# Kernel optimization log

Measured on AMD Instinct MI355X. Metric: run time of the kernel, lower is better.

The kernel has to match this reference:

```python
import jax, jax.numpy as jnp
import numpy as np
import math

K = 10      # number of propagation steps
BETA = 2.0  # log-weighting base
N_NODES = 100000
N_EDGES = 1000000
HIDDEN = 64


def setup_inputs() -> dict:
    key = jax.random.key(0)
    k1, k2, k3 = jax.random.split(key, 3)
    feat = jax.random.normal(k1, (N_NODES, HIDDEN), dtype=jnp.float32)
    src = jax.random.randint(k2, (N_EDGES,), 0, N_NODES, dtype=jnp.int64)
    dst = jax.random.randint(k3, (N_EDGES,), 0, N_NODES, dtype=jnp.int64)
    return {"feat": feat, "src": src, "dst": dst}


def reference(feat, src, dst):
    n = feat.shape[0]
    ones_e = jnp.ones(src.shape, dtype=feat.dtype)
    # out-degree of source nodes, in-degree of destination nodes
    out_deg = jax.ops.segment_sum(ones_e, src, num_segments=n)
    in_deg = jax.ops.segment_sum(ones_e, dst, num_segments=n)
    src_norm = jnp.maximum(out_deg, 1.0) ** -0.5  # [N]
    dst_norm = jnp.maximum(in_deg, 1.0) ** -0.5   # [N]

    # log-based combination weights over the K+1 snapshots
    logs = [math.log(BETA + i) for i in range(1, K + 2)]
    denom = sum(logs)
    w = [l / denom for l in logs]

    h = feat
    out = w[0] * feat
    for step in range(K):
        # gather-scale on source side, scatter-sum to destinations, scale on dst side
        m = (h * src_norm[:, None])[src]                      # [E, D]
        h = jax.ops.segment_sum(m, dst, num_segments=n)       # [N, D]
        h = h * dst_norm[:, None]
        out = out + w[step + 1] * h
    return out
```

## Files before the change

kernel.cpp:

```cpp
#include <hip/hip_runtime.h>
#include <hip/hip_bf16.h>
#include <math.h>

#define HIDDEN 64
#define K_STEPS 10
#define SLICES 2
#define SLICE_N 51200
#define SLICE_W (SLICE_N / 4)
#define PADU 4

struct Wts { float v[K_STEPS + 1]; };

typedef float v2f __attribute__((ext_vector_type(2)));

__device__ __forceinline__ float bits2f(unsigned int u) {
    union { unsigned int i; float f; } c; c.i = u; return c.f;
}
__device__ __forceinline__ unsigned short f2bf(float f) {
    union { float f; unsigned int u; } c; c.f = f;
    unsigned int u = c.u;
    return (unsigned short)((u + 0x7FFF + ((u >> 16) & 1)) >> 16);
}
__device__ __forceinline__ void unpack_add(v2f acc[4], uint4 v) {
    v2f t;
    t.x = bits2f(v.x << 16); t.y = bits2f(v.x & 0xFFFF0000u); acc[0] += t;
    t.x = bits2f(v.y << 16); t.y = bits2f(v.y & 0xFFFF0000u); acc[1] += t;
    t.x = bits2f(v.z << 16); t.y = bits2f(v.z & 0xFFFF0000u); acc[2] += t;
    t.x = bits2f(v.w << 16); t.y = bits2f(v.w & 0xFFFF0000u); acc[3] += t;
}

__global__ void detect_kernel(const int* __restrict__ srcw,
                              const unsigned short* __restrict__ featw,
                              int* __restrict__ flags) {
    __shared__ int odd_nonzero;
    __shared__ int exp_in_range;
    if (threadIdx.x == 0) { odd_nonzero = 0; exp_in_range = 0; }
    __syncthreads();
    int w = srcw[2 * threadIdx.x + 1];
    if (w != 0) atomicAdd(&odd_nonzero, 1);
    unsigned short f = featw[2 * threadIdx.x];
    int ex = (f >> 7) & 0xFF;
    if (ex >= 90 && ex <= 135) atomicAdd(&exp_in_range, 1);
    __syncthreads();
    if (threadIdx.x == 0) {
        flags[0] = (odd_nonzero == 0) ? 1 : 0;
        flags[1] = (exp_in_range >= 240) ? 0 : 1;
    }
}

__global__ void hist_kernel(const void* __restrict__ src, const void* __restrict__ dst,
                            const int* __restrict__ flags,
                            unsigned* __restrict__ partials,
                            unsigned char* __restrict__ rank,
                            int E, int chunkE, int nchunks) {
    __shared__ unsigned bins[SLICE_W];
    int cx = blockIdx.x, sy = blockIdx.y, az = blockIdx.z;
    for (int i = threadIdx.x; i < SLICE_W; i += 256) bins[i] = 0;
    __syncthreads();
    const void* arr = az ? dst : src;
    int i64 = flags[0];
    int base = cx * chunkE;
    int lim = min(base + chunkE, E);
    int sliceBase = sy * SLICE_N;
    for (int e = base + threadIdx.x; e < lim; e += 256) {
        int v = i64 ? (int)((const long long*)arr)[e] : ((const int*)arr)[e];
        unsigned local = (unsigned)(v - sliceBase);
        if (local < SLICE_N) {
            int sh = (local & 3) * 8;
            unsigned old = atomicAdd(&bins[local >> 2], 1u << sh);
            if (az) rank[e] = (unsigned char)((old >> sh) & 0xFF);
        }
    }
    __syncthreads();
    unsigned* out = partials + ((size_t)((az * SLICES + sy) * nchunks + cx)) * SLICE_W;
    for (int i = threadIdx.x; i < SLICE_W; i += 256) out[i] = bins[i];
}

__global__ void reduce_kernel(const unsigned* __restrict__ partials,
                              unsigned* __restrict__ chunk_pre,
                              int* __restrict__ out_deg, int* __restrict__ in_deg,
                              float* __restrict__ src_norm, float* __restrict__ dst_norm,
                              int N, int nchunks) {
    int t = blockIdx.x * blockDim.x + threadIdx.x;
    if (t >= 2 * SLICES * SLICE_W) return;
    int a = t / (SLICES * SLICE_W);
    int r = t % (SLICES * SLICE_W);
    int s = r / SLICE_W;
    int lw = r % SLICE_W;
    const unsigned* p = partials + ((size_t)((a * SLICES + s) * nchunks)) * SLICE_W + lw;
    unsigned sum = 0;
    if (a == 1) {
        for (int c = 0; c < nchunks; ++c) {
            chunk_pre[((size_t)(c * SLICES + s)) * SLICE_W + lw] = sum;
            sum += p[(size_t)c * SLICE_W];
        }
    } else {
        for (int c = 0; c < nchunks; ++c) sum += p[(size_t)c * SLICE_W];
    }
    int nodeBase = s * SLICE_N + lw * 4;
    int* deg = a ? in_deg : out_deg;
    float* nrm = a ? dst_norm : src_norm;
    #pragma unroll
    for (int k = 0; k < 4; ++k) {
        int n = nodeBase + k;
        if (n < N) {
            int d = (int)((sum >> (k * 8)) & 0xFF);
            deg[n] = d;
            nrm[n] = 1.0f / sqrtf(fmaxf((float)d, 1.0f));
        }
    }
}

__global__ void scanA_kernel(const int* __restrict__ deg, int* __restrict__ row_ptr,
                             int* __restrict__ block_sums, int N) {
    __shared__ int lds[256];
    int t = threadIdx.x;
    int base = blockIdx.x * 1024 + t * 4;
    int v0 = (base + 0 < N) ? ((deg[base + 0] + (PADU - 1)) & ~(PADU - 1)) : 0;
    int v1 = (base + 1 < N) ? ((deg[base + 1] + (PADU - 1)) & ~(PADU - 1)) : 0;
    int v2 = (base + 2 < N) ? ((deg[base + 2] + (PADU - 1)) & ~(PADU - 1)) : 0;
    int v3 = (base + 3 < N) ? ((deg[base + 3] + (PADU - 1)) & ~(PADU - 1)) : 0;
    int s = v0 + v1 + v2 + v3;
    lds[t] = s;
    __syncthreads();
    for (int off = 1; off < 256; off <<= 1) {
        int x = 0;
        if (t >= off) x = lds[t - off];
        __syncthreads();
        if (t >= off) lds[t] += x;
        __syncthreads();
    }
    int excl = lds[t] - s;
    if (t == 255) block_sums[blockIdx.x] = lds[255];
    if (base + 0 < N) row_ptr[base + 0] = excl;
    if (base + 1 < N) row_ptr[base + 1] = excl + v0;
    if (base + 2 < N) row_ptr[base + 2] = excl + v0 + v1;
    if (base + 3 < N) row_ptr[base + 3] = excl + v0 + v1 + v2;
}

__global__ void scanB_kernel(int* __restrict__ bs, int nb) {
    __shared__ int lds[1024];
    int t = threadIdx.x;
    int v = (t < nb) ? bs[t] : 0;
    lds[t] = v;
    __syncthreads();
    for (int off = 1; off < 1024; off <<= 1) {
        int x = 0;
        if (t >= off) x = lds[t - off];
        __syncthreads();
        if (t >= off) lds[t] += x;
        __syncthreads();
    }
    if (t < nb) bs[t] = lds[t] - v;
    if (t == nb - 1) bs[1024] = lds[t];
}

__global__ void scanC_pad_kernel(const int* __restrict__ raw_row,
                                 const int* __restrict__ block_offs,
                                 const int* __restrict__ in_deg,
                                 int* __restrict__ row_fin,
                                 int* __restrict__ col, int N) {
    int i = blockIdx.x * blockDim.x + threadIdx.x;
    if (i >= N) return;
    int b0 = raw_row[i] + block_offs[i >> 10];
    int b1 = (i + 1 < N) ? (raw_row[i + 1] + block_offs[(i + 1) >> 10])
                         : block_offs[1024];
    row_fin[i] = b0;
    if (i == 0) row_fin[N] = block_offs[1024];
    int s = b0 + in_deg[i];
    for (int j = s; j < b1; ++j) col[j] = N;
}

__global__ void scatter_kernel(const void* __restrict__ src, const void* __restrict__ dst,
                               const int* __restrict__ flags,
                               const int* __restrict__ row_fin,
                               const unsigned* __restrict__ chunk_pre,
                               const unsigned char* __restrict__ rank,
                               int* __restrict__ col, int E, int chunkShift) {
    int i64 = flags[0];
    int stride = gridDim.x * blockDim.x;
    for (int e = blockIdx.x * blockDim.x + threadIdx.x; e < E; e += stride) {
        int s, d;
        if (i64) { s = (int)((const long long*)src)[e]; d = (int)((const long long*)dst)[e]; }
        else     { s = ((const int*)src)[e];            d = ((const int*)dst)[e]; }
        int c = e >> chunkShift;
        int si = (d >= SLICE_N) ? 1 : 0;
        unsigned local = (unsigned)d - si * SLICE_N;
        unsigned prew = chunk_pre[((size_t)(c * SLICES + si)) * SLICE_W + (local >> 2)];
        int pre = (int)((prew >> ((local & 3) * 8)) & 0xFF);
        col[row_fin[d] + pre + (int)rank[e]] = s;
    }
}

__global__ void init_kernel(const void* __restrict__ feat_raw,
                            const int* __restrict__ flags,
                            const float* __restrict__ src_norm,
                            uint4* __restrict__ hs8, float4* __restrict__ out_acc4,
                            float w0, int nchunks, int writeAcc) {
    int i = blockIdx.x * blockDim.x + threadIdx.x;
    if (i >= nchunks) return;
    int n = i >> 3;
    int c = i & 7;
    float sn = src_norm[n];
    float f[8];
    if (flags[1]) {
        float4 a = ((const float4*)feat_raw)[i * 2];
        float4 b = ((const float4*)feat_raw)[i * 2 + 1];
        f[0] = a.x; f[1] = a.y; f[2] = a.z; f[3] = a.w;
        f[4] = b.x; f[5] = b.y; f[6] = b.z; f[7] = b.w;
    } else {
        uint4 u = ((const uint4*)feat_raw)[i];
        f[0] = bits2f(u.x << 16); f[1] = bits2f(u.x & 0xFFFF0000u);
        f[2] = bits2f(u.y << 16); f[3] = bits2f(u.y & 0xFFFF0000u);
        f[4] = bits2f(u.z << 16); f[5] = bits2f(u.z & 0xFFFF0000u);
        f[6] = bits2f(u.w << 16); f[7] = bits2f(u.w & 0xFFFF0000u);
    }
    uint4 h;
    h.x = (unsigned int)f2bf(f[0] * sn) | ((unsigned int)f2bf(f[1] * sn) << 16);
    h.y = (unsigned int)f2bf(f[2] * sn) | ((unsigned int)f2bf(f[3] * sn) << 16);
    h.z = (unsigned int)f2bf(f[4] * sn) | ((unsigned int)f2bf(f[5] * sn) << 16);
    h.w = (unsigned int)f2bf(f[6] * sn) | ((unsigned int)f2bf(f[7] * sn) << 16);
    hs8[i] = h;
    if (writeAcc) {
        float4 o0, o1;
        o0.x = w0 * f[0]; o0.y = w0 * f[1]; o0.z = w0 * f[2]; o0.w = w0 * f[3];
        o1.x = w0 * f[4]; o1.y = w0 * f[5]; o1.z = w0 * f[6]; o1.w = w0 * f[7];
        size_t ob = (size_t)n * 16 + c * 2;
        out_acc4[ob] = o0;
        out_acc4[ob + 1] = o1;
    }
}

__global__ void zrow_kernel(uint4* __restrict__ hs_region, int snapN, int nsnap, int N) {
    int i = blockIdx.x * blockDim.x + threadIdx.x;
    int k = i >> 3, r = i & 7;
    if (k < nsnap) {
        uint4 z; z.x = 0u; z.y = 0u; z.z = 0u; z.w = 0u;
        hs_region[(size_t)k * snapN + ((size_t)N << 3) + r] = z;
    }
}

__device__ __forceinline__ void gather_row(const uint4* __restrict__ hs8,
                                           const int* __restrict__ col,
                                           int beg, int end, int fo,
                                           v2f a0[4], v2f a1[4]) {
    int e = beg;
    int nq = (end - beg) >> 2;
    if (nq & 1) {
        int4 c = *(const int4*)(col + e);
        uint4 v0 = hs8[((unsigned)c.x << 3) | fo];
        uint4 v1 = hs8[((unsigned)c.y << 3) | fo];
        uint4 v2 = hs8[((unsigned)c.z << 3) | fo];
        uint4 v3 = hs8[((unsigned)c.w << 3) | fo];
        unpack_add(a0, v0);
        unpack_add(a1, v1);
        unpack_add(a0, v2);
        unpack_add(a1, v3);
        e += 4;
    }
    if (e < end) {
        int4 c0 = *(const int4*)(col + e);
        int4 c1 = *(const int4*)(col + e + 4);
        for (;;) {
            int4 d0 = c0, d1 = c1;
            int ne = e + 8;
            if (ne < end) {
                c0 = *(const int4*)(col + ne);
                c1 = *(const int4*)(col + ne + 4);
            }
            uint4 v0 = hs8[((unsigned)d0.x << 3) | fo];
            uint4 v1 = hs8[((unsigned)d0.y << 3) | fo];
            uint4 v2 = hs8[((unsigned)d0.z << 3) | fo];
            uint4 v3 = hs8[((unsigned)d0.w << 3) | fo];
            uint4 v4 = hs8[((unsigned)d1.x << 3) | fo];
            uint4 v5 = hs8[((unsigned)d1.y << 3) | fo];
            uint4 v6 = hs8[((unsigned)d1.z << 3) | fo];
            uint4 v7 = hs8[((unsigned)d1.w << 3) | fo];
            unpack_add(a0, v0);
            unpack_add(a1, v1);
            unpack_add(a0, v2);
            unpack_add(a1, v3);
            unpack_add(a0, v4);
            unpack_add(a1, v5);
            unpack_add(a0, v6);
            unpack_add(a1, v7);
            e = ne;
            if (e >= end) break;
        }
    }
}

__global__ __launch_bounds__(256) void step_snap(
        const uint4* __restrict__ hs8, const int* __restrict__ row_fin,
        const int* __restrict__ col, const float* __restrict__ src_norm,
        const float* __restrict__ dst_norm, uint4* __restrict__ hs_next8, int N) {
    int wid = (blockIdx.x * 256 + threadIdx.x) >> 6;
    int nw = (gridDim.x * 256) >> 6;
    int lane = threadIdx.x & 63;
    int grp = lane >> 3, fo = lane & 7;
    for (int nbase = wid * 8; nbase < N; nbase += nw * 8) {
        int node = nbase + grp;
        int beg = 0, end = 0;
        if (node < N) { beg = row_fin[node]; end = row_fin[node + 1]; }
        v2f a0[4] = {v2f{0.f,0.f}, v2f{0.f,0.f}, v2f{0.f,0.f}, v2f{0.f,0.f}};
        v2f a1[4] = {v2f{0.f,0.f}, v2f{0.f,0.f}, v2f{0.f,0.f}, v2f{0.f,0.f}};
        if (beg < end) gather_row(hs8, col, beg, end, fo, a0, a1);
        if (node < N) {
            float m = dst_norm[node] * src_norm[node];
            #pragma unroll
            for (int k = 0; k < 4; ++k) a0[k] += a1[k];
            uint4 hn;
            hn.x = (unsigned int)f2bf(a0[0].x * m) | ((unsigned int)f2bf(a0[0].y * m) << 16);
            hn.y = (unsigned int)f2bf(a0[1].x * m) | ((unsigned int)f2bf(a0[1].y * m) << 16);
            hn.z = (unsigned int)f2bf(a0[2].x * m) | ((unsigned int)f2bf(a0[2].y * m) << 16);
            hn.w = (unsigned int)f2bf(a0[3].x * m) | ((unsigned int)f2bf(a0[3].y * m) << 16);
            hs_next8[((unsigned)node << 3) | fo] = hn;
        }
    }
}

template <bool LAST>
__global__ __launch_bounds__(256) void step_acc(
        const uint4* __restrict__ hs8, const int* __restrict__ row_fin,
        const int* __restrict__ col, const float* __restrict__ src_norm,
        const float* __restrict__ dst_norm, uint4* __restrict__ hs_next8,
        float4* __restrict__ out_acc4, float4* __restrict__ out4, float w, int N) {
    int wid = (blockIdx.x * 256 + threadIdx.x) >> 6;
    int nw = (gridDim.x * 256) >> 6;
    int lane = threadIdx.x & 63;
    int grp = lane >> 3, fo = lane & 7;
    for (int nbase = wid * 8; nbase < N; nbase += nw * 8) {
        int node = nbase + grp;
        int beg = 0, end = 0;
        if (node < N) { beg = row_fin[node]; end = row_fin[node + 1]; }
        v2f a0[4] = {v2f{0.f,0.f}, v2f{0.f,0.f}, v2f{0.f,0.f}, v2f{0.f,0.f}};
        v2f a1[4] = {v2f{0.f,0.f}, v2f{0.f,0.f}, v2f{0.f,0.f}, v2f{0.f,0.f}};
        if (beg < end) gather_row(hs8, col, beg, end, fo, a0, a1);
        if (node < N) {
            #pragma unroll
            for (int k = 0; k < 4; ++k) a0[k] += a1[k];
            float dn = dst_norm[node];
            float h0 = a0[0].x * dn, h1 = a0[0].y * dn, h2 = a0[1].x * dn, h3 = a0[1].y * dn;
            float h4 = a0[2].x * dn, h5 = a0[2].y * dn, h6 = a0[3].x * dn, h7 = a0[3].y * dn;
            size_t ob = (size_t)node * 16 + fo * 2;
            float4 o0 = out_acc4[ob];
            float4 o1 = out_acc4[ob + 1];
            o0.x += w * h0; o0.y += w * h1; o0.z += w * h2; o0.w += w * h3;
            o1.x += w * h4; o1.y += w * h5; o1.z += w * h6; o1.w += w * h7;
            if (LAST) {
                out4[ob] = o0;
                out4[ob + 1] = o1;
            } else {
                out_acc4[ob] = o0;
                out_acc4[ob + 1] = o1;
                float sn = src_norm[node];
                uint4 hn;
                hn.x = (unsigned int)f2bf(h0 * sn) | ((unsigned int)f2bf(h1 * sn) << 16);
                hn.y = (unsigned int)f2bf(h2 * sn) | ((unsigned int)f2bf(h3 * sn) << 16);
                hn.z = (unsigned int)f2bf(h4 * sn) | ((unsigned int)f2bf(h5 * sn) << 16);
                hn.w = (unsigned int)f2bf(h6 * sn) | ((unsigned int)f2bf(h7 * sn) << 16);
                hs_next8[((unsigned)node << 3) | fo] = hn;
            }
        }
    }
}

__global__ void combine_kernel(const void* __restrict__ feat_raw,
                               const int* __restrict__ flags,
                               const int* __restrict__ out_deg,
                               const uint4* __restrict__ hs_base,
                               float4* __restrict__ out4,
                               Wts wts, int snapN, int nchunks) {
    int i = blockIdx.x * blockDim.x + threadIdx.x;
    if (i >= nchunks) return;
    int n = i >> 3;
    float inv = sqrtf(fmaxf((float)out_deg[n], 1.0f));
    float acc[8];
    if (flags[1]) {
        float4 a = ((const float4*)feat_raw)[i * 2];
        float4 b = ((const float4*)feat_raw)[i * 2 + 1];
        acc[0] = a.x; acc[1] = a.y; acc[2] = a.z; acc[3] = a.w;
        acc[4] = b.x; acc[5] = b.y; acc[6] = b.z; acc[7] = b.w;
    } else {
        uint4 u = ((const uint4*)feat_raw)[i];
        acc[0] = bits2f(u.x << 16); acc[1] = bits2f(u.x & 0xFFFF0000u);
        acc[2] = bits2f(u.y << 16); acc[3] = bits2f(u.y & 0xFFFF0000u);
        acc[4] = bits2f(u.z << 16); acc[5] = bits2f(u.z & 0xFFFF0000u);
        acc[6] = bits2f(u.w << 16); acc[7] = bits2f(u.w & 0xFFFF0000u);
    }
    float w0 = wts.v[0];
    #pragma unroll
    for (int j = 0; j < 8; ++j) acc[j] *= w0;
    #pragma unroll
    for (int k = 1; k <= K_STEPS; ++k) {
        uint4 u = hs_base[(size_t)k * snapN + i];
        float s = wts.v[k] * inv;
        acc[0] += s * bits2f(u.x << 16); acc[1] += s * bits2f(u.x & 0xFFFF0000u);
        acc[2] += s * bits2f(u.y << 16); acc[3] += s * bits2f(u.y & 0xFFFF0000u);
        acc[4] += s * bits2f(u.z << 16); acc[5] += s * bits2f(u.z & 0xFFFF0000u);
        acc[6] += s * bits2f(u.w << 16); acc[7] += s * bits2f(u.w & 0xFFFF0000u);
    }
    float4 o0 = {acc[0], acc[1], acc[2], acc[3]};
    float4 o1 = {acc[4], acc[5], acc[6], acc[7]};
    out4[i * 2] = o0;
    out4[i * 2 + 1] = o1;
}

extern "C" void kernel_launch(void* const* d_in, const int* in_sizes, int n_in,
                              void* d_out, int out_size, void* d_ws, size_t ws_size,
                              hipStream_t stream) {
    const void* feat_raw = d_in[0];
    const void* src_raw = d_in[1];
    const void* dst_raw = d_in[2];
    float4* out4 = (float4*)d_out;

    const int N = in_sizes[0] / HIDDEN;
    const int E = (in_sizes[1] > 1500000) ? in_sizes[1] / 2 : in_sizes[1];
    const int nchunks = N * 8;
    const int snapN = nchunks + 8;
    const int Ecap = E + (PADU - 1) * N + 16;

    auto align256 = [](size_t b) { return (b + 255) & ~(size_t)255; };
    size_t base_bytes = align256(2 * sizeof(int))
                      + align256((size_t)N * sizeof(int))
                      + align256((size_t)N * sizeof(int))
                      + align256((size_t)(N + 1) * sizeof(int))
                      + align256((size_t)(N + 1) * sizeof(int))
                      + align256(1025 * sizeof(int))
                      + align256((size_t)Ecap * sizeof(int))
                      + align256((size_t)N * sizeof(float))
                      + align256((size_t)N * sizeof(float))
                      + align256((size_t)E);
    auto hist_bytes = [&](int C) {
        return align256((size_t)2 * SLICES * C * SLICE_W * sizeof(unsigned))
             + align256((size_t)C * SLICES * SLICE_W * sizeof(unsigned));
    };
    size_t snap_bytes = align256((size_t)(K_STEPS + 1) * snapN * sizeof(uint4));
    size_t acc_bytes  = align256((size_t)2 * snapN * sizeof(uint4))
                      + align256((size_t)N * 16 * sizeof(float4));

    int chunkShift = 13;
    int CHc = (E + (1 << chunkShift) - 1) >> chunkShift;
    int snapMode;
    if (ws_size >= base_bytes + hist_bytes(CHc) + snap_bytes) {
        snapMode = 1;
    } else {
        chunkShift = 14;
        CHc = (E + (1 << chunkShift) - 1) >> chunkShift;
        if (ws_size >= base_bytes + hist_bytes(CHc) + snap_bytes) {
            snapMode = 1;
        } else if (ws_size >= base_bytes + hist_bytes(CHc) + acc_bytes) {
            snapMode = 0;
        } else {
            chunkShift = 15;
            CHc = (E + (1 << chunkShift) - 1) >> chunkShift;
            snapMode = 0;
        }
    }
    const int chunkE = 1 << chunkShift;

    char* p = (char*)d_ws;
    auto alloc = [&](size_t bytes) {
        char* r = p;
        p += (bytes + 255) & ~(size_t)255;
        return r;
    };
    int* flags = (int*)alloc(2 * sizeof(int));
    int* out_deg = (int*)alloc((size_t)N * sizeof(int));
    int* in_deg = (int*)alloc((size_t)N * sizeof(int));
    int* row_ptr = (int*)alloc((size_t)(N + 1) * sizeof(int));
    int* row_fin = (int*)alloc((size_t)(N + 1) * sizeof(int));
    int* block_sums = (int*)alloc(1025 * sizeof(int));
    int* col = (int*)alloc((size_t)Ecap * sizeof(int));
    float* src_norm = (float*)alloc((size_t)N * sizeof(float));
    float* dst_norm = (float*)alloc((size_t)N * sizeof(float));
    unsigned char* rank = (unsigned char*)alloc((size_t)E);
    unsigned* partials = (unsigned*)alloc((size_t)2 * SLICES * CHc * SLICE_W * sizeof(unsigned));
    unsigned* chunk_pre = (unsigned*)alloc((size_t)CHc * SLICES * SLICE_W * sizeof(unsigned));
    uint4* hs_region;
    float4* out_acc = nullptr;
    if (snapMode) {
        hs_region = (uint4*)alloc((size_t)(K_STEPS + 1) * snapN * sizeof(uint4));
    } else {
        hs_region = (uint4*)alloc((size_t)2 * snapN * sizeof(uint4));
        out_acc = (float4*)alloc((size_t)N * 16 * sizeof(float4));
    }

    double logs[K_STEPS + 1];
    double denom = 0.0;
    for (int i = 0; i < K_STEPS + 1; ++i) {
        logs[i] = log(2.0 + (double)(i + 1));
        denom += logs[i];
    }
    Wts wts;
    for (int i = 0; i < K_STEPS + 1; ++i) wts.v[i] = (float)(logs[i] / denom);

    detect_kernel<<<1, 256, 0, stream>>>((const int*)src_raw,
                                         (const unsigned short*)feat_raw, flags);
    hist_kernel<<<dim3(CHc, SLICES, 2), 256, 0, stream>>>(src_raw, dst_raw, flags,
                                                          partials, rank, E, chunkE, CHc);
    reduce_kernel<<<(2 * SLICES * SLICE_W + 255) / 256, 256, 0, stream>>>(
        partials, chunk_pre, out_deg, in_deg, src_norm, dst_norm, N, CHc);

    int nb = (N + 1023) / 1024;
    scanA_kernel<<<nb, 256, 0, stream>>>(in_deg, row_ptr, block_sums, N);
    scanB_kernel<<<1, 1024, 0, stream>>>(block_sums, nb);
    scanC_pad_kernel<<<(N + 255) / 256, 256, 0, stream>>>(row_ptr, block_sums, in_deg,
                                                          row_fin, col, N);
    scatter_kernel<<<min(2048, (E + 255) / 256), 256, 0, stream>>>(
        src_raw, dst_raw, flags, row_fin, chunk_pre, rank, col, E, chunkShift);

    init_kernel<<<(nchunks + 255) / 256, 256, 0, stream>>>(
        feat_raw, flags, src_norm, hs_region, out_acc, wts.v[0], nchunks, snapMode ? 0 : 1);
    zrow_kernel<<<1, 128, 0, stream>>>(hs_region, snapN, snapMode ? (K_STEPS + 1) : 2, N);

    const int work_blocks = (((N + 7) / 8) + 3) / 4;
    if (snapMode) {
        for (int step = 0; step < K_STEPS; ++step) {
            const uint4* cur = hs_region + (size_t)step * snapN;
            uint4* nxt = hs_region + (size_t)(step + 1) * snapN;
            step_snap<<<work_blocks, 256, 0, stream>>>(cur, row_fin, col, src_norm,
                                                       dst_norm, nxt, N);
        }
        combine_kernel<<<(nchunks + 255) / 256, 256, 0, stream>>>(
            feat_raw, flags, out_deg, hs_region, out4, wts, snapN, nchunks);
    } else {
        uint4* cur = hs_region;
        uint4* nxt = hs_region + snapN;
        for (int step = 0; step < K_STEPS; ++step) {
            if (step == K_STEPS - 1) {
                step_acc<true><<<work_blocks, 256, 0, stream>>>(
                    cur, row_fin, col, src_norm, dst_norm, nxt, out_acc, out4,
                    wts.v[step + 1], N);
            } else {
                step_acc<false><<<work_blocks, 256, 0, stream>>>(
                    cur, row_fin, col, src_norm, dst_norm, nxt, out_acc, out4,
                    wts.v[step + 1], N);
            }
            uint4* t = cur; cur = nxt; nxt = t;
        }
    }
}
```

Before: 390.9 us.

## Use single full-range LDS histogram per block and fold zero-row init into init kernel

The degree histogram now covers all 102400 nodes in one 100KB LDS array per block with 1024 threads, instead of two 51200-node slices processed by separate blocks. Each edge index is read once per array rather than once per slice, and the bounds check and slice arithmetic disappear from the histogram and scatter kernels. The separate zero-row kernel is merged into init_kernel, saving one launch. In exchange, the large LDS footprint limits occupancy to one block per CU, and the hard-coded FULLN assumes N is at most 102400.

```diff
diff --git a/kernel.cpp b/kernel.cpp
--- a/kernel.cpp
+++ b/kernel.cpp
@@ -4,9 +4,8 @@
 
 #define HIDDEN 64
 #define K_STEPS 10
-#define SLICES 2
-#define SLICE_N 51200
-#define SLICE_W (SLICE_N / 4)
+#define FULLN 102400
+#define FULLW (FULLN / 4)
 #define PADU 4
 
 struct Wts { float v[K_STEPS + 1]; };
@@ -48,32 +47,30 @@
     }
 }
 
-__global__ void hist_kernel(const void* __restrict__ src, const void* __restrict__ dst,
-                            const int* __restrict__ flags,
-                            unsigned* __restrict__ partials,
-                            unsigned char* __restrict__ rank,
-                            int E, int chunkE, int nchunks) {
-    __shared__ unsigned bins[SLICE_W];
-    int cx = blockIdx.x, sy = blockIdx.y, az = blockIdx.z;
-    for (int i = threadIdx.x; i < SLICE_W; i += 256) bins[i] = 0;
+__global__ __launch_bounds__(1024) void hist_kernel(
+        const void* __restrict__ src, const void* __restrict__ dst,
+        const int* __restrict__ flags,
+        unsigned* __restrict__ partials,
+        unsigned char* __restrict__ rank,
+        int E, int chunkE, int nchunks) {
+    __shared__ unsigned bins[FULLW];
+    int cx = blockIdx.x, az = blockIdx.y;
+    for (int i = threadIdx.x; i < FULLW; i += 1024) bins[i] = 0;
     __syncthreads();
     const void* arr = az ? dst : src;
     int i64 = flags[0];
     int base = cx * chunkE;
     int lim = min(base + chunkE, E);
-    int sliceBase = sy * SLICE_N;
-    for (int e = base + threadIdx.x; e < lim; e += 256) {
+    for (int e = base + threadIdx.x; e < lim; e += 1024) {
         int v = i64 ? (int)((const long long*)arr)[e] : ((const int*)arr)[e];
-        unsigned local = (unsigned)(v - sliceBase);
-        if (local < SLICE_N) {
-            int sh = (local & 3) * 8;
-            unsigned old = atomicAdd(&bins[local >> 2], 1u << sh);
-            if (az) rank[e] = (unsigned char)((old >> sh) & 0xFF);
-        }
+        unsigned uv = (unsigned)v;
+        int sh = (uv & 3) * 8;
+        unsigned old = atomicAdd(&bins[uv >> 2], 1u << sh);
+        if (az) rank[e] = (unsigned char)((old >> sh) & 0xFF);
     }
     __syncthreads();
-    unsigned* out = partials + ((size_t)((az * SLICES + sy) * nchunks + cx)) * SLICE_W;
-    for (int i = threadIdx.x; i < SLICE_W; i += 256) out[i] = bins[i];
+    unsigned* out = partials + ((size_t)(az * nchunks + cx)) * FULLW;
+    for (int i = threadIdx.x; i < FULLW; i += 1024) out[i] = bins[i];
 }
 
 __global__ void reduce_kernel(const unsigned* __restrict__ partials,
@@ -82,22 +79,20 @@
                               float* __restrict__ src_norm, float* __restrict__ dst_norm,
                               int N, int nchunks) {
     int t = blockIdx.x * blockDim.x + threadIdx.x;
-    if (t >= 2 * SLICES * SLICE_W) return;
-    int a = t / (SLICES * SLICE_W);
-    int r = t % (SLICES * SLICE_W);
-    int s = r / SLICE_W;
-    int lw = r % SLICE_W;
-    const unsigned* p = partials + ((size_t)((a * SLICES + s) * nchunks)) * SLICE_W + lw;
+    if (t >= 2 * FULLW) return;
+    int a = t / FULLW;
+    int lw = t % FULLW;
+    const unsigned* p = partials + ((size_t)a * nchunks) * FULLW + lw;
     unsigned sum = 0;
     if (a == 1) {
         for (int c = 0; c < nchunks; ++c) {
-            chunk_pre[((size_t)(c * SLICES + s)) * SLICE_W + lw] = sum;
-            sum += p[(size_t)c * SLICE_W];
+            chunk_pre[(size_t)c * FULLW + lw] = sum;
+            sum += p[(size_t)c * FULLW];
         }
     } else {
-        for (int c = 0; c < nchunks; ++c) sum += p[(size_t)c * SLICE_W];
-    }
-    int nodeBase = s * SLICE_N + lw * 4;
+        for (int c = 0; c < nchunks; ++c) sum += p[(size_t)c * FULLW];
+    }
+    int nodeBase = lw * 4;
     int* deg = a ? in_deg : out_deg;
     float* nrm = a ? dst_norm : src_norm;
     #pragma unroll
@@ -184,10 +179,8 @@
         if (i64) { s = (int)((const long long*)src)[e]; d = (int)((const long long*)dst)[e]; }
         else     { s = ((const int*)src)[e];            d = ((const int*)dst)[e]; }
         int c = e >> chunkShift;
-        int si = (d >= SLICE_N) ? 1 : 0;
-        unsigned local = (unsigned)d - si * SLICE_N;
-        unsigned prew = chunk_pre[((size_t)(c * SLICES + si)) * SLICE_W + (local >> 2)];
-        int pre = (int)((prew >> ((local & 3) * 8)) & 0xFF);
+        unsigned prew = chunk_pre[(size_t)c * FULLW + ((unsigned)d >> 2)];
+        int pre = (int)((prew >> ((d & 3) * 8)) & 0xFF);
         col[row_fin[d] + pre + (int)rank[e]] = s;
     }
 }
@@ -196,9 +189,18 @@
                             const int* __restrict__ flags,
                             const float* __restrict__ src_norm,
                             uint4* __restrict__ hs8, float4* __restrict__ out_acc4,
-                            float w0, int nchunks, int writeAcc) {
+                            float w0, int nchunks, int writeAcc,
+                            int snapN, int nsnap) {
     int i = blockIdx.x * blockDim.x + threadIdx.x;
-    if (i >= nchunks) return;
+    if (i >= nchunks) {
+        int j = i - nchunks;
+        int k = j >> 3, r = j & 7;
+        if (k < nsnap) {
+            uint4 z; z.x = 0u; z.y = 0u; z.z = 0u; z.w = 0u;
+            hs8[(size_t)k * snapN + nchunks + r] = z;
+        }
+        return;
+    }
     int n = i >> 3;
     int c = i & 7;
     float sn = src_norm[n];
@@ -228,15 +230,6 @@
         size_t ob = (size_t)n * 16 + c * 2;
         out_acc4[ob] = o0;
         out_acc4[ob + 1] = o1;
-    }
-}
-
-__global__ void zrow_kernel(uint4* __restrict__ hs_region, int snapN, int nsnap, int N) {
-    int i = blockIdx.x * blockDim.x + threadIdx.x;
-    int k = i >> 3, r = i & 7;
-    if (k < nsnap) {
-        uint4 z; z.x = 0u; z.y = 0u; z.z = 0u; z.w = 0u;
-        hs_region[(size_t)k * snapN + ((size_t)N << 3) + r] = z;
     }
 }
 
@@ -432,8 +425,8 @@
                       + align256((size_t)N * sizeof(float))
                       + align256((size_t)E);
     auto hist_bytes = [&](int C) {
-        return align256((size_t)2 * SLICES * C * SLICE_W * sizeof(unsigned))
-             + align256((size_t)C * SLICES * SLICE_W * sizeof(unsigned));
+        return align256((size_t)2 * C * FULLW * sizeof(unsigned))
+             + align256((size_t)C * FULLW * sizeof(unsigned));
     };
     size_t snap_bytes = align256((size_t)(K_STEPS + 1) * snapN * sizeof(uint4));
     size_t acc_bytes  = align256((size_t)2 * snapN * sizeof(uint4))
@@ -475,8 +468,8 @@
     float* src_norm = (float*)alloc((size_t)N * sizeof(float));
     float* dst_norm = (float*)alloc((size_t)N * sizeof(float));
     unsigned char* rank = (unsigned char*)alloc((size_t)E);
-    unsigned* partials = (unsigned*)alloc((size_t)2 * SLICES * CHc * SLICE_W * sizeof(unsigned));
-    unsigned* chunk_pre = (unsigned*)alloc((size_t)CHc * SLICES * SLICE_W * sizeof(unsigned));
+    unsigned* partials = (unsigned*)alloc((size_t)2 * CHc * FULLW * sizeof(unsigned));
+    unsigned* chunk_pre = (unsigned*)alloc((size_t)CHc * FULLW * sizeof(unsigned));
     uint4* hs_region;
     float4* out_acc = nullptr;
     if (snapMode) {
@@ -497,9 +490,9 @@
 
     detect_kernel<<<1, 256, 0, stream>>>((const int*)src_raw,
                                          (const unsigned short*)feat_raw, flags);
-    hist_kernel<<<dim3(CHc, SLICES, 2), 256, 0, stream>>>(src_raw, dst_raw, flags,
-                                                          partials, rank, E, chunkE, CHc);
-    reduce_kernel<<<(2 * SLICES * SLICE_W + 255) / 256, 256, 0, stream>>>(
+    hist_kernel<<<dim3(CHc, 2), 1024, 0, stream>>>(src_raw, dst_raw, flags,
+                                                   partials, rank, E, chunkE, CHc);
+    reduce_kernel<<<(2 * FULLW + 255) / 256, 256, 0, stream>>>(
         partials, chunk_pre, out_deg, in_deg, src_norm, dst_norm, N, CHc);
 
     int nb = (N + 1023) / 1024;
@@ -510,9 +503,10 @@
     scatter_kernel<<<min(2048, (E + 255) / 256), 256, 0, stream>>>(
         src_raw, dst_raw, flags, row_fin, chunk_pre, rank, col, E, chunkShift);
 
-    init_kernel<<<(nchunks + 255) / 256, 256, 0, stream>>>(
-        feat_raw, flags, src_norm, hs_region, out_acc, wts.v[0], nchunks, snapMode ? 0 : 1);
-    zrow_kernel<<<1, 128, 0, stream>>>(hs_region, snapN, snapMode ? (K_STEPS + 1) : 2, N);
+    const int nsnap = snapMode ? (K_STEPS + 1) : 2;
+    init_kernel<<<(nchunks + nsnap * 8 + 255) / 256, 256, 0, stream>>>(
+        feat_raw, flags, src_norm, hs_region, out_acc, wts.v[0], nchunks,
+        snapMode ? 0 : 1, snapN, nsnap);
 
     const int work_blocks = (((N + 7) / 8) + 3) / 4;
     if (snapMode) {
```

After: 376.7 us. -3.6%, faster.
